# Kernel tuning notes

Measured on AMD Instinct MI355X. Metric: run time of the kernel, lower is better.

Reference implementation:

```python
import jax, jax.numpy as jnp
import numpy as np


def setup_inputs() -> dict:
    key = jax.random.key(0)
    k1, k2 = jax.random.split(key)
    B, N, M, D = 4, 8192, 8192, 3
    pc1 = jax.random.normal(k1, (B, N, D), dtype=jnp.float32)
    pc2 = jax.random.normal(k2, (B, M, D), dtype=jnp.float32)
    return {"pc1": pc1, "pc2": pc2}


def _chamfer_one(a, b):
    # a: [N, 3], b: [M, 3]
    # squared pairwise distances via ||a||^2 + ||b||^2 - 2 a.b (avoids [N,M,3] intermediate)
    a2 = jnp.sum(a * a, axis=-1)          # [N]
    b2 = jnp.sum(b * b, axis=-1)          # [M]
    d2 = a2[:, None] + b2[None, :] - 2.0 * jnp.einsum('nd,md->nm', a, b)  # [N, M]
    d2 = jnp.maximum(d2, 0.0)
    # bidirectional nearest-neighbor min-reduction, averaged per direction
    return jnp.mean(jnp.min(d2, axis=1)) + jnp.mean(jnp.min(d2, axis=0))


def reference(pc1, pc2):
    # transpose_mode=False: points already [N, d]. Per-batch scalar chamfer distance.
    D = jax.vmap(_chamfer_one)(pc1.astype(jnp.float32), pc2.astype(jnp.float32))  # [B]
    return jnp.squeeze(D)
```

## Files before the change

kernel.cpp:

```cpp
#include <hip/hip_runtime.h>
#include <hip/hip_fp16.h>
#include <math.h>


#define BATCH   4
#define NPTS    8192
#define THREADS 256
#define NCHUNKS 32
#define MSLICES 8
#define MSL     1024
#define SC      256.0f
#define ISC     (1.0f/256.0f)
#define FLT_BIG 3.4e38f

typedef _Float16 half8 __attribute__((ext_vector_type(8)));
typedef float f32x16 __attribute__((ext_vector_type(16)));

union U4H8 { uint4 u; half8 h; };

__device__ __forceinline__ unsigned pk(__half lo, __half hi) {
    return (unsigned)__half_as_ushort(lo) | ((unsigned)__half_as_ushort(hi) << 16);
}

__global__ __launch_bounds__(THREADS) void chamfer_mfma_kernel(
        const float* __restrict__ pc1, const float* __restrict__ pc2,
        float* __restrict__ part, float* __restrict__ out) {
    const int bid    = blockIdx.x;
    const int slice  = bid & 7;
    const int nchunk = (bid >> 3) & 31;
    const int batch  = (bid >> 8) & 3;
    const int dir    = bid >> 10;

    if (bid == 0 && threadIdx.x < BATCH) out[threadIdx.x] = 0.0f;

    const float* acld = dir ? pc2 : pc1;
    const float* bcld = dir ? pc1 : pc2;

    __shared__ unsigned smem[8448];

    const int t = threadIdx.x;
    const int L = t & 63;
    const int w = t >> 6;

    const float* bb = bcld + ((size_t)batch * NPTS + (size_t)slice * MSL) * 3;
    #pragma unroll
    for (int k = 0; k < 4; ++k) {
        const int p = k * THREADS + t;
        const float x = bb[3 * p + 0], y = bb[3 * p + 1], z = bb[3 * p + 2];
        __half hx = __float2half(x), hy = __float2half(y), hz = __float2half(z);
        __half lx = __float2half((x - __half2float(hx)) * SC);
        __half ly = __float2half((y - __half2float(hy)) * SC);
        __half lz = __float2half((z - __half2float(hz)) * SC);
        __half sx = __float2half(__half2float(hx) * ISC);
        __half sy = __float2half(__half2float(hy) * ISC);
        __half sz = __float2half(__half2float(hz) * ISC);
        const float b2 = fmaf(x, x, fmaf(y, y, z * z));
        __half hb2 = __float2half(b2);
        __half lb2 = __float2half(b2 - __half2float(hb2));
        __half zer = __float2half(0.0f);
        uint4* g0 = (uint4*)&smem[p * 4];
        uint4* g1 = (uint4*)&smem[4096 + p * 4];
        *g0 = make_uint4(pk(hx, hy), pk(hz, sx), pk(sy, sz), pk(hb2, zer));
        *g1 = make_uint4(pk(lx, ly), pk(lz, lb2), 0u, 0u);
    }

    const int g = L >> 5;
    const __half one = __float2half(1.0f);
    const __half hz0 = __float2half(0.0f);
    U4H8 A[2];
    #pragma unroll
    for (int ti = 0; ti < 2; ++ti) {
        const int n = nchunk * 256 + w * 64 + (L & 31) + ti * 32;
        const float* ap = acld + ((size_t)batch * NPTS + n) * 3;
        const float vx = -2.0f * ap[0], vy = -2.0f * ap[1], vz = -2.0f * ap[2];
        __half hx = __float2half(vx), hy = __float2half(vy), hzv = __float2half(vz);
        __half lx = __float2half((vx - __half2float(hx)) * SC);
        __half ly = __float2half((vy - __half2float(hy)) * SC);
        __half lz = __float2half((vz - __half2float(hzv)) * SC);
        __half sx = __float2half(__half2float(hx) * ISC);
        __half sy = __float2half(__half2float(hy) * ISC);
        __half sz = __float2half(__half2float(hzv) * ISC);
        if (g == 0) {
            A[ti].u = make_uint4(pk(hx, hy), pk(hzv, lx), pk(ly, lz), pk(one, hz0));
        } else {
            A[ti].u = make_uint4(pk(sx, sy), pk(sz, one), 0u, 0u);
        }
    }

    __syncthreads();

    const f32x16 zf = {0.0f};
    float rm0[16], rm1[16];
    #pragma unroll
    for (int r = 0; r < 16; ++r) { rm0[r] = FLT_BIG; rm1[r] = FLT_BIG; }

    const int rbase = g * 4096 + (L & 31) * 4;
    for (int mt = 0; mt < 32; mt += 2) {
        U4H8 b0, b1;
        b0.u = *(const uint4*)&smem[rbase + mt * 128];
        b1.u = *(const uint4*)&smem[rbase + mt * 128 + 128];
        f32x16 d0a = __builtin_amdgcn_mfma_f32_32x32x16_f16(A[0].h, b0.h, zf, 0, 0, 0);
        f32x16 d1a = __builtin_amdgcn_mfma_f32_32x32x16_f16(A[1].h, b0.h, zf, 0, 0, 0);
        f32x16 d0b = __builtin_amdgcn_mfma_f32_32x32x16_f16(A[0].h, b1.h, zf, 0, 0, 0);
        f32x16 d1b = __builtin_amdgcn_mfma_f32_32x32x16_f16(A[1].h, b1.h, zf, 0, 0, 0);
        #pragma unroll
        for (int r = 0; r < 16; ++r) {
            rm0[r] = fminf(fminf(rm0[r], d0a[r]), d0b[r]);
            rm1[r] = fminf(fminf(rm1[r], d1a[r]), d1b[r]);
        }
    }

    __syncthreads();
    float* sf = (float*)smem;
    const int wbase = w * 2112;
    #pragma unroll
    for (int r = 0; r < 16; ++r) {
        const int row0 = (r & 3) + 8 * (r >> 2) + 4 * g;
        sf[wbase + row0 * 33 + (L & 31)] = rm0[r];
        sf[wbase + (row0 + 32) * 33 + (L & 31)] = rm1[r];
    }
    __syncthreads();

    float v = FLT_BIG;
    const int rb = wbase + L * 33;
    #pragma unroll
    for (int i = 0; i < 32; ++i) v = fminf(v, sf[rb + i]);

    const int grow = nchunk * 256 + w * 64 + L;
    part[(((size_t)dir * BATCH + batch) * MSLICES + slice) * NPTS + grow] = v;
}

__global__ __launch_bounds__(THREADS) void chamfer_reduce_kernel(
        const float* __restrict__ pc1, const float* __restrict__ pc2,
        const float* __restrict__ part, float* __restrict__ out) {
    const int idx   = blockIdx.x * THREADS + threadIdx.x;
    const int n     = idx & (NPTS - 1);
    const int batch = (idx >> 13) & 3;
    const int dir   = idx >> 15;

    const float* pb = part + (((size_t)dir * BATCH + batch) * MSLICES) * NPTS + n;
    float v = pb[0];
    #pragma unroll
    for (int s = 1; s < MSLICES; ++s) v = fminf(v, pb[(size_t)s * NPTS]);

    const float* acld = dir ? pc2 : pc1;
    const float* ap = acld + ((size_t)batch * NPTS + n) * 3;
    const float x = ap[0], y = ap[1], z = ap[2];
    const float a2 = fmaf(x, x, fmaf(y, y, z * z));
    float d2 = fmaxf(v + a2, 0.0f);

    #pragma unroll
    for (int off = 32; off > 0; off >>= 1)
        d2 += __shfl_down(d2, off, 64);

    __shared__ float wsum[THREADS / 64];
    if ((threadIdx.x & 63) == 0) wsum[threadIdx.x >> 6] = d2;
    __syncthreads();

    if (threadIdx.x == 0) {
        float ssum = 0.0f;
        #pragma unroll
        for (int wv = 0; wv < THREADS / 64; ++wv) ssum += wsum[wv];
        atomicAdd(&out[batch], ssum * (1.0f / (float)NPTS));
    }
}

extern "C" void kernel_launch(void* const* d_in, const int* in_sizes, int n_in,
                              void* d_out, int out_size, void* d_ws, size_t ws_size,
                              hipStream_t stream) {
    const float* pc1 = (const float*)d_in[0];
    const float* pc2 = (const float*)d_in[1];
    float* out  = (float*)d_out;
    float* part = (float*)d_ws;

    chamfer_mfma_kernel<<<2 * BATCH * NCHUNKS * MSLICES, THREADS, 0, stream>>>(
        pc1, pc2, part, out);
    chamfer_reduce_kernel<<<(2 * BATCH * NPTS) / THREADS, THREADS, 0, stream>>>(
        pc1, pc2, part, out);
}
```

Measured before the change: 84.98 us.

## Compute both chamfer directions from one distance matrix pass

Drops the second, transposed pass over the distance matrix. Each tile now yields both row minima and column minima, and the a2 and b2 norms are folded into the MFMA operands so the tile holds full squared distances. Column minima are reduced across lanes with a shuffle, then merged with shared-memory atomicMin on order-preserving encoded floats and written as per-chunk partials. This halves the MFMA work and the grid size, at the cost of extra min operations, shuffles and LDS atomics in the inner loop and a larger column-partial buffer (32 chunks) for the reduce kernel to read.

```diff
diff --git a/kernel.cpp b/kernel.cpp
--- a/kernel.cpp
+++ b/kernel.cpp
@@ -21,28 +21,37 @@
 __device__ __forceinline__ unsigned pk(__half lo, __half hi) {
     return (unsigned)__half_as_ushort(lo) | ((unsigned)__half_as_ushort(hi) << 16);
 }
+__device__ __forceinline__ unsigned enc_f32(float f) {
+    unsigned b = __float_as_uint(f);
+    return (b & 0x80000000u) ? ~b : (b | 0x80000000u);
+}
+__device__ __forceinline__ float dec_f32(unsigned k) {
+    unsigned b = (k & 0x80000000u) ? (k & 0x7FFFFFFFu) : ~k;
+    return __uint_as_float(b);
+}
 
 __global__ __launch_bounds__(THREADS) void chamfer_mfma_kernel(
         const float* __restrict__ pc1, const float* __restrict__ pc2,
-        float* __restrict__ part, float* __restrict__ out) {
+        float* __restrict__ part_row, float* __restrict__ part_col,
+        float* __restrict__ out) {
     const int bid    = blockIdx.x;
-    const int slice  = bid & 7;
+    const int mslice = bid & 7;
     const int nchunk = (bid >> 3) & 31;
-    const int batch  = (bid >> 8) & 3;
-    const int dir    = bid >> 10;
+    const int batch  = bid >> 8;
 
     if (bid == 0 && threadIdx.x < BATCH) out[threadIdx.x] = 0.0f;
 
-    const float* acld = dir ? pc2 : pc1;
-    const float* bcld = dir ? pc1 : pc2;
-
-    __shared__ unsigned smem[8448];
+    __shared__ unsigned smem[9472];
+    unsigned* colmin = &smem[8448];
 
     const int t = threadIdx.x;
     const int L = t & 63;
     const int w = t >> 6;
-
-    const float* bb = bcld + ((size_t)batch * NPTS + (size_t)slice * MSL) * 3;
+    const int g = L >> 5;
+    const __half one = __float2half(1.0f);
+    const __half z0  = __float2half(0.0f);
+
+    const float* bb = pc2 + ((size_t)batch * NPTS + (size_t)mslice * MSL) * 3;
     #pragma unroll
     for (int k = 0; k < 4; ++k) {
         const int p = k * THREADS + t;
@@ -57,33 +66,35 @@
         const float b2 = fmaf(x, x, fmaf(y, y, z * z));
         __half hb2 = __float2half(b2);
         __half lb2 = __float2half(b2 - __half2float(hb2));
-        __half zer = __float2half(0.0f);
         uint4* g0 = (uint4*)&smem[p * 4];
         uint4* g1 = (uint4*)&smem[4096 + p * 4];
-        *g0 = make_uint4(pk(hx, hy), pk(hz, sx), pk(sy, sz), pk(hb2, zer));
-        *g1 = make_uint4(pk(lx, ly), pk(lz, lb2), 0u, 0u);
-    }
-
-    const int g = L >> 5;
-    const __half one = __float2half(1.0f);
-    const __half hz0 = __float2half(0.0f);
+        *g0 = make_uint4(pk(hx, hy), pk(hz, sx), pk(sy, sz), pk(one, hb2));
+        *g1 = make_uint4(pk(lx, ly), pk(lz, one), pk(lb2, z0), pk(z0, z0));
+    }
+    #pragma unroll
+    for (int i = 0; i < 4; ++i) colmin[i * THREADS + t] = 0xFFFFFFFFu;
+
     U4H8 A[2];
     #pragma unroll
     for (int ti = 0; ti < 2; ++ti) {
         const int n = nchunk * 256 + w * 64 + (L & 31) + ti * 32;
-        const float* ap = acld + ((size_t)batch * NPTS + n) * 3;
-        const float vx = -2.0f * ap[0], vy = -2.0f * ap[1], vz = -2.0f * ap[2];
-        __half hx = __float2half(vx), hy = __float2half(vy), hzv = __float2half(vz);
-        __half lx = __float2half((vx - __half2float(hx)) * SC);
-        __half ly = __float2half((vy - __half2float(hy)) * SC);
-        __half lz = __float2half((vz - __half2float(hzv)) * SC);
-        __half sx = __float2half(__half2float(hx) * ISC);
-        __half sy = __float2half(__half2float(hy) * ISC);
-        __half sz = __float2half(__half2float(hzv) * ISC);
+        const float* ap = pc1 + ((size_t)batch * NPTS + n) * 3;
+        const float x = ap[0], y = ap[1], z = ap[2];
+        const float vx = -2.0f * x, vy = -2.0f * y, vz = -2.0f * z;
+        __half Hx = __float2half(vx), Hy = __float2half(vy), Hz = __float2half(vz);
+        __half Lx = __float2half((vx - __half2float(Hx)) * SC);
+        __half Ly = __float2half((vy - __half2float(Hy)) * SC);
+        __half Lz = __float2half((vz - __half2float(Hz)) * SC);
+        __half Sx = __float2half(__half2float(Hx) * ISC);
+        __half Sy = __float2half(__half2float(Hy) * ISC);
+        __half Sz = __float2half(__half2float(Hz) * ISC);
+        const float a2 = fmaf(x, x, fmaf(y, y, z * z));
+        __half ha2 = __float2half(a2);
+        __half la2 = __float2half(a2 - __half2float(ha2));
         if (g == 0) {
-            A[ti].u = make_uint4(pk(hx, hy), pk(hzv, lx), pk(ly, lz), pk(one, hz0));
+            A[ti].u = make_uint4(pk(Hx, Hy), pk(Hz, Lx), pk(Ly, Lz), pk(ha2, one));
         } else {
-            A[ti].u = make_uint4(pk(sx, sy), pk(sz, one), 0u, 0u);
+            A[ti].u = make_uint4(pk(Sx, Sy), pk(Sz, la2), pk(one, z0), pk(z0, z0));
         }
     }
 
@@ -103,11 +114,18 @@
         f32x16 d1a = __builtin_amdgcn_mfma_f32_32x32x16_f16(A[1].h, b0.h, zf, 0, 0, 0);
         f32x16 d0b = __builtin_amdgcn_mfma_f32_32x32x16_f16(A[0].h, b1.h, zf, 0, 0, 0);
         f32x16 d1b = __builtin_amdgcn_mfma_f32_32x32x16_f16(A[1].h, b1.h, zf, 0, 0, 0);
+        float c0 = FLT_BIG, c1 = FLT_BIG;
         #pragma unroll
         for (int r = 0; r < 16; ++r) {
             rm0[r] = fminf(fminf(rm0[r], d0a[r]), d0b[r]);
             rm1[r] = fminf(fminf(rm1[r], d1a[r]), d1b[r]);
+            c0 = fminf(fminf(c0, d0a[r]), d1a[r]);
+            c1 = fminf(fminf(c1, d0b[r]), d1b[r]);
         }
+        c0 = fminf(c0, __shfl_xor(c0, 32, 64));
+        c1 = fminf(c1, __shfl_xor(c1, 32, 64));
+        const float cv = (L < 32) ? c0 : c1;
+        atomicMin(&colmin[mt * 32 + L], enc_f32(cv));
     }
 
     __syncthreads();
@@ -125,29 +143,36 @@
     const int rb = wbase + L * 33;
     #pragma unroll
     for (int i = 0; i < 32; ++i) v = fminf(v, sf[rb + i]);
-
     const int grow = nchunk * 256 + w * 64 + L;
-    part[(((size_t)dir * BATCH + batch) * MSLICES + slice) * NPTS + grow] = v;
+    part_row[((size_t)batch * MSLICES + mslice) * NPTS + grow] = v;
+
+    #pragma unroll
+    for (int i = 0; i < 4; ++i) {
+        const int j = i * THREADS + t;
+        part_col[((size_t)batch * NCHUNKS + nchunk) * NPTS + mslice * MSL + j] =
+            dec_f32(colmin[j]);
+    }
 }
 
 __global__ __launch_bounds__(THREADS) void chamfer_reduce_kernel(
-        const float* __restrict__ pc1, const float* __restrict__ pc2,
-        const float* __restrict__ part, float* __restrict__ out) {
+        const float* __restrict__ part_row, const float* __restrict__ part_col,
+        float* __restrict__ out) {
     const int idx   = blockIdx.x * THREADS + threadIdx.x;
+    const int dir   = idx >> 15;
+    const int batch = (idx >> 13) & 3;
     const int n     = idx & (NPTS - 1);
-    const int batch = (idx >> 13) & 3;
-    const int dir   = idx >> 15;
-
-    const float* pb = part + (((size_t)dir * BATCH + batch) * MSLICES) * NPTS + n;
-    float v = pb[0];
-    #pragma unroll
-    for (int s = 1; s < MSLICES; ++s) v = fminf(v, pb[(size_t)s * NPTS]);
-
-    const float* acld = dir ? pc2 : pc1;
-    const float* ap = acld + ((size_t)batch * NPTS + n) * 3;
-    const float x = ap[0], y = ap[1], z = ap[2];
-    const float a2 = fmaf(x, x, fmaf(y, y, z * z));
-    float d2 = fmaxf(v + a2, 0.0f);
+
+    float v = FLT_BIG;
+    if (dir == 0) {
+        const float* pb = part_row + (size_t)batch * MSLICES * NPTS + n;
+        #pragma unroll
+        for (int s = 0; s < MSLICES; ++s) v = fminf(v, pb[(size_t)s * NPTS]);
+    } else {
+        const float* pb = part_col + (size_t)batch * NCHUNKS * NPTS + n;
+        #pragma unroll
+        for (int s = 0; s < NCHUNKS; ++s) v = fminf(v, pb[(size_t)s * NPTS]);
+    }
+    float d2 = fmaxf(v, 0.0f);
 
     #pragma unroll
     for (int off = 32; off > 0; off >>= 1)
@@ -170,11 +195,12 @@
                               hipStream_t stream) {
     const float* pc1 = (const float*)d_in[0];
     const float* pc2 = (const float*)d_in[1];
-    float* out  = (float*)d_out;
-    float* part = (float*)d_ws;
-
-    chamfer_mfma_kernel<<<2 * BATCH * NCHUNKS * MSLICES, THREADS, 0, stream>>>(
-        pc1, pc2, part, out);
+    float* out      = (float*)d_out;
+    float* part_row = (float*)d_ws;
+    float* part_col = part_row + (size_t)BATCH * MSLICES * NPTS;
+
+    chamfer_mfma_kernel<<<BATCH * NCHUNKS * MSLICES, THREADS, 0, stream>>>(
+        pc1, pc2, part_row, part_col, out);
     chamfer_reduce_kernel<<<(2 * BATCH * NPTS) / THREADS, THREADS, 0, stream>>>(
-        pc1, pc2, part, out);
-}
+        part_row, part_col, out);
+}
```

New measurement: 79.18 us. -6.8%, faster.
